# Optimization experiments

Measured on AMD Instinct MI355X. Metric: run time of the kernel, lower is better.

Reference implementation:

```python
import jax, jax.numpy as jnp
import numpy as np

INFEAT = 4096
OUTFEAT = 11008
TOKENS = 2048


def setup_inputs() -> dict:
    key = jax.random.key(0)
    k1, k2, k3, k4, k5 = jax.random.split(key, 5)
    x = jax.random.normal(k1, (TOKENS, INFEAT), dtype=jnp.float32)
    # Random uint8 int-weights, packed 4-per-uint32 exactly like pack():
    # word = w1 | w2<<8 | w3<<16 | w4<<24, rows grouped along infeatures.
    wbytes = jax.random.randint(k2, (INFEAT // 4, 4, OUTFEAT), 0, 256, dtype=jnp.int32).astype(jnp.uint32)
    qweight = (wbytes[:, 0] | (wbytes[:, 1] << 8) | (wbytes[:, 2] << 16) | (wbytes[:, 3] << 24))
    qweight = qweight.astype(jnp.int32)  # same bit pattern as uint32 buffer
    scales = (jax.random.uniform(k3, (OUTFEAT,), dtype=jnp.float32) * 0.01 + 1e-4)
    zeros = jax.random.randint(k4, (OUTFEAT,), 0, 256, dtype=jnp.int32)  # uint8 zero points
    bias = jax.random.normal(k5, (OUTFEAT,), dtype=jnp.float32) * 0.01
    return {"x": x, "qweight": qweight, "scales": scales, "zeros": zeros, "bias": bias}


def _dequant(qweight, scales, zeros):
    q = qweight.astype(jnp.uint32)  # [INFEAT//4, OUTFEAT]
    b0 = (q & 0xFF)
    b1 = ((q >> 8) & 0xFF)
    b2 = ((q >> 16) & 0xFF)
    b3 = ((q >> 24) & 0xFF)
    w_int = jnp.stack([b0, b1, b2, b3], axis=1).reshape(-1, q.shape[-1])  # [INFEAT, OUTFEAT]
    # pack(): int = round(w/scale) + zero  =>  w = (int - zero) * scale (per output channel)
    return (w_int.astype(jnp.float32) - zeros.astype(jnp.float32)[None, :]) * scales[None, :]


def reference(x, qweight, scales, zeros, bias):
    w = _dequant(qweight, scales, zeros)          # [INFEAT, OUTFEAT]
    return x @ w + bias[None, :]                  # [TOKENS, OUTFEAT]
```

## Files before the change

kernel.cpp:

```cpp
#include <hip/hip_runtime.h>
#include <hip/hip_bf16.h>

#define INFEAT 4096
#define OUTFEAT 11008
#define TOKENS 2048

typedef int v4i __attribute__((ext_vector_type(4)));
typedef __bf16 bf16_t;
typedef bf16_t bf16x4 __attribute__((ext_vector_type(4)));
typedef bf16_t bf16x8 __attribute__((ext_vector_type(8)));
typedef float f32x4 __attribute__((ext_vector_type(4)));

__device__ __forceinline__ void async_copy16(const void* g, void* l) {
    __builtin_amdgcn_global_load_lds((const __attribute__((address_space(1))) void*)g,
                                     (__attribute__((address_space(3))) void*)l,
                                     16, 0, 0);
}

__global__ __launch_bounds__(256) void quant_x(
    const float* __restrict__ x, unsigned int* __restrict__ xq,
    float* __restrict__ xscale, int* __restrict__ xsum)
{
    __shared__ float smax[4];
    __shared__ int ssum[4];
    const int row = blockIdx.x;
    const int tid = threadIdx.x;
    const int lane = tid & 63, wid = tid >> 6;
    const float* xr = x + (size_t)row * INFEAT;

    float4 v[4];
    #pragma unroll
    for (int i = 0; i < 4; ++i) v[i] = *(const float4*)&xr[tid * 16 + i * 4];

    float am = 0.f;
    #pragma unroll
    for (int i = 0; i < 4; ++i)
        am = fmaxf(am, fmaxf(fmaxf(fabsf(v[i].x), fabsf(v[i].y)),
                             fmaxf(fabsf(v[i].z), fabsf(v[i].w))));
    #pragma unroll
    for (int o = 32; o > 0; o >>= 1) am = fmaxf(am, __shfl_xor(am, o, 64));
    if (lane == 0) smax[wid] = am;
    __syncthreads();
    am = fmaxf(fmaxf(smax[0], smax[1]), fmaxf(smax[2], smax[3]));
    const float inv = am > 0.f ? 127.0f / am : 0.f;
    const float sc  = am > 0.f ? am / 127.0f : 0.f;

    int lsum = 0;
    unsigned int pk[4];
    #pragma unroll
    for (int i = 0; i < 4; ++i) {
        int q0 = (int)rintf(fminf(fmaxf(v[i].x * inv, -127.f), 127.f));
        int q1 = (int)rintf(fminf(fmaxf(v[i].y * inv, -127.f), 127.f));
        int q2 = (int)rintf(fminf(fmaxf(v[i].z * inv, -127.f), 127.f));
        int q3 = (int)rintf(fminf(fmaxf(v[i].w * inv, -127.f), 127.f));
        lsum += q0 + q1 + q2 + q3;
        pk[i] = (q0 & 255) | ((q1 & 255) << 8) | ((q2 & 255) << 16) | ((unsigned)(q3 & 255) << 24);
    }
    *(uint4*)&xq[(size_t)row * (INFEAT / 4) + tid * 4] = *(uint4*)pk;

    #pragma unroll
    for (int o = 32; o > 0; o >>= 1) lsum += __shfl_xor(lsum, o, 64);
    if (lane == 0) ssum[wid] = lsum;
    __syncthreads();
    if (tid == 0) {
        xsum[row] = ssum[0] + ssum[1] + ssum[2] + ssum[3];
        xscale[row] = sc;
    }
}

__global__ __launch_bounds__(256) void t_w(
    const unsigned int* __restrict__ qw, unsigned char* __restrict__ wt)
{
    __shared__ unsigned int Tw[64 * 64];
    const int n0 = blockIdx.x * 64;
    const int kp0 = blockIdx.y * 64;
    const int tn = threadIdx.x & 63;
    const int tk4 = threadIdx.x >> 6;

    #pragma unroll
    for (int it = 0; it < 16; ++it) {
        const int kp = tk4 * 16 + it;
        const unsigned int q = qw[(size_t)(kp0 + kp) * OUTFEAT + n0 + tn] ^ 0x80808080u;
        const int slot = (kp >> 2) ^ (tn & 15);
        Tw[tn * 64 + slot * 4 + (kp & 3)] = q;
    }
    __syncthreads();

    #pragma unroll
    for (int i = 0; i < 4; ++i) {
        const int flat = i * 256 + threadIdx.x;
        const int n = flat >> 4;
        const int c = flat & 15;
        uint4 v = *(const uint4*)&Tw[n * 64 + ((c ^ (n & 15)) * 4)];
        *(uint4*)&wt[(size_t)(n0 + n) * INFEAT + (size_t)kp0 * 4 + c * 16] = v;
    }
}

__global__ __launch_bounds__(256, 4) void q3gemm_i8(
    const unsigned char* __restrict__ xqb, const unsigned char* __restrict__ wt,
    const float* __restrict__ scales, const int* __restrict__ zeros,
    const float* __restrict__ bias, const float* __restrict__ xscale,
    const int* __restrict__ xsum, float* __restrict__ out)
{
    __shared__ unsigned char Als[128 * 128];
    __shared__ unsigned char Bls[128 * 128];

    const int tid = threadIdx.x;
    const int n0 = (blockIdx.x >> 4) * 128;
    const int m0 = (blockIdx.x & 15) * 128;

    const int wid = tid >> 6, lane = tid & 63;
    const int wm = (wid & 1) * 64, wn = (wid >> 1) * 64;
    const int lr = lane & 15, lq = lane >> 4;

    const int rb0  = wid * 32;
    const int rsub = lane >> 3;
    const int sl   = lane & 7;

    v4i acc[4][4];
    #pragma unroll
    for (int i = 0; i < 4; ++i)
        #pragma unroll
        for (int j = 0; j < 4; ++j)
            acc[i][j] = (v4i){0, 0, 0, 0};

    for (int kt = 0; kt < INFEAT / 128; ++kt) {
        const int k0 = kt * 128;

        #pragma unroll
        for (int p = 0; p < 4; ++p) {
            const int r = rb0 + p * 8 + rsub;
            const int s = sl ^ (r & 7);
            async_copy16(&xqb[(size_t)(m0 + r) * INFEAT + k0 + s * 16], Als + (rb0 + p * 8) * 128);
        }
        #pragma unroll
        for (int p = 0; p < 4; ++p) {
            const int r = rb0 + p * 8 + rsub;
            const int s = sl ^ (r & 7);
            async_copy16(&wt[(size_t)(n0 + r) * INFEAT + k0 + s * 16], Bls + (rb0 + p * 8) * 128);
        }

        __syncthreads();

        #pragma unroll
        for (int ks = 0; ks < 2; ++ks) {
            v4i af[4], bfv[4];
            #pragma unroll
            for (int t = 0; t < 4; ++t) {
                const int ra = wm + t * 16 + lr;
                const int pa = (ks * 4 + lq) ^ (ra & 7);
                af[t] = *(const v4i*)&Als[ra * 128 + pa * 16];
                const int rb = wn + t * 16 + lr;
                const int pb = (ks * 4 + lq) ^ (rb & 7);
                bfv[t] = *(const v4i*)&Bls[rb * 128 + pb * 16];
            }
            #pragma unroll
            for (int i = 0; i < 4; ++i)
                #pragma unroll
                for (int j = 0; j < 4; ++j)
                    acc[i][j] = __builtin_amdgcn_mfma_i32_16x16x64_i8(af[i], bfv[j], acc[i][j], 0, 0, 0);
        }

        __syncthreads();
    }

    #pragma unroll
    for (int j = 0; j < 4; ++j) {
        const int col = n0 + wn + j * 16 + lr;
        const float sn = scales[col];
        const int zi = 128 - zeros[col];
        const float bv = bias[col];
        #pragma unroll
        for (int i = 0; i < 4; ++i) {
            const int rb = m0 + wm + i * 16 + lq * 4;
            #pragma unroll
            for (int r = 0; r < 4; ++r) {
                const int tot = acc[i][j][r] + zi * xsum[rb + r];
                out[(size_t)(rb + r) * OUTFEAT + col] = xscale[rb + r] * sn * (float)tot + bv;
            }
        }
    }
}

#define LDSS 72
__global__ __launch_bounds__(256) void q3gemm_fb(
    const float* __restrict__ x, const unsigned int* __restrict__ qw,
    const float* __restrict__ scales, const int* __restrict__ zeros,
    const float* __restrict__ bias, float* __restrict__ out)
{
    __shared__ bf16_t Als[128 * LDSS];
    __shared__ bf16_t Bls[128 * LDSS];
    const int tid = threadIdx.x;
    const int m0 = blockIdx.y * 128;
    const int n0 = blockIdx.x * 128;
    const int bcol = tid & 127;
    const int bpr  = tid >> 7;
    const float scf = scales[n0 + bcol];
    const float nzs = (float)zeros[n0 + bcol] * scf;
    const int acolg = tid & 15;
    const int arow0 = tid >> 4;
    const int wid  = tid >> 6;
    const int lane = tid & 63;
    const int wm = (wid & 1) * 64;
    const int wn = (wid >> 1) * 64;
    const int lr = lane & 15;
    const int lq = lane >> 4;
    f32x4 acc[4][4];
    #pragma unroll
    for (int i = 0; i < 4; ++i)
        #pragma unroll
        for (int j = 0; j < 4; ++j) acc[i][j] = (f32x4)0.0f;
    for (int kt = 0; kt < INFEAT / 64; ++kt) {
        const int k0 = kt * 64;
        #pragma unroll
        for (int p = 0; p < 8; ++p) {
            const int row = arow0 + p * 16;
            const float4 v = *(const float4*)&x[(size_t)(m0 + row) * INFEAT + k0 + acolg * 4];
            bf16x4 b;
            b[0] = (bf16_t)v.x; b[1] = (bf16_t)v.y; b[2] = (bf16_t)v.z; b[3] = (bf16_t)v.w;
            *(bf16x4*)&Als[row * LDSS + acolg * 4] = b;
        }
        const int kp0 = k0 >> 2;
        #pragma unroll
        for (int it = 0; it < 8; ++it) {
            const int prel = it * 2 + bpr;
            const unsigned int q = qw[(size_t)(kp0 + prel) * OUTFEAT + n0 + bcol];
            bf16x4 b;
            b[0] = (bf16_t)((float)(q & 0xFFu)        * scf - nzs);
            b[1] = (bf16_t)((float)((q >> 8) & 0xFFu) * scf - nzs);
            b[2] = (bf16_t)((float)((q >> 16) & 0xFFu)* scf - nzs);
            b[3] = (bf16_t)((float)(q >> 24)          * scf - nzs);
            *(bf16x4*)&Bls[bcol * LDSS + prel * 4] = b;
        }
        __syncthreads();
        #pragma unroll
        for (int ks = 0; ks < 2; ++ks) {
            bf16x8 af[4], bfv[4];
            #pragma unroll
            for (int t = 0; t < 4; ++t) {
                af[t]  = *(const bf16x8*)&Als[(wm + t * 16 + lr) * LDSS + ks * 32 + lq * 8];
                bfv[t] = *(const bf16x8*)&Bls[(wn + t * 16 + lr) * LDSS + ks * 32 + lq * 8];
            }
            #pragma unroll
            for (int i = 0; i < 4; ++i)
                #pragma unroll
                for (int j = 0; j < 4; ++j)
                    acc[i][j] = __builtin_amdgcn_mfma_f32_16x16x32_bf16(af[i], bfv[j], acc[i][j], 0, 0, 0);
        }
        __syncthreads();
    }
    #pragma unroll
    for (int j = 0; j < 4; ++j) {
        const int col = n0 + wn + j * 16 + lr;
        const float bv = bias[col];
        #pragma unroll
        for (int i = 0; i < 4; ++i) {
            const int rbs = m0 + wm + i * 16 + lq * 4;
            #pragma unroll
            for (int r = 0; r < 4; ++r)
                out[(size_t)(rbs + r) * OUTFEAT + col] = acc[i][j][r] + bv;
        }
    }
}

extern "C" void kernel_launch(void* const* d_in, const int* in_sizes, int n_in,
                              void* d_out, int out_size, void* d_ws, size_t ws_size,
                              hipStream_t stream) {
    const float*        x      = (const float*)d_in[0];
    const unsigned int* qw     = (const unsigned int*)d_in[1];
    const float*        scales = (const float*)d_in[2];
    const int*          zeros  = (const int*)d_in[3];
    const float*        bias   = (const float*)d_in[4];
    float*              out    = (float*)d_out;

    const size_t wt_bytes = (size_t)OUTFEAT * INFEAT;
    const size_t xq_bytes = (size_t)TOKENS * INFEAT;
    const size_t need = wt_bytes + xq_bytes + TOKENS * (sizeof(float) + sizeof(int)) + 256;

    if (ws_size >= need) {
        unsigned char* wt = (unsigned char*)d_ws;
        unsigned int* xq  = (unsigned int*)((char*)d_ws + wt_bytes);
        float* xscale = (float*)((char*)d_ws + wt_bytes + xq_bytes);
        int*   xsum   = (int*)((char*)d_ws + wt_bytes + xq_bytes + TOKENS * sizeof(float));

        quant_x<<<dim3(TOKENS), dim3(256), 0, stream>>>(x, xq, xscale, xsum);
        t_w<<<dim3(OUTFEAT / 64, (INFEAT / 4) / 64), dim3(256), 0, stream>>>(qw, wt);
        q3gemm_i8<<<dim3((OUTFEAT / 128) * (TOKENS / 128)), dim3(256), 0, stream>>>(
            (const unsigned char*)xq, wt, scales, zeros, bias, xscale, xsum, out);
    } else {
        q3gemm_fb<<<dim3(OUTFEAT / 128, TOKENS / 128), dim3(256), 0, stream>>>(
            x, qw, scales, zeros, bias, out);
    }
}
```

Measured before the change: 297.6 us.

## Fuse weight transpose into int8 GEMM B-tile load, drop t_w kernel

Removes the separate weight transpose kernel and its 45MB workspace round trip. The GEMM now reads packed qweight words directly from global memory into registers, flips the sign bits, and writes them transposed into the swizzled LDS B tile. This saves one kernel launch and a full write plus re-read of the transposed weight. In exchange, B loads become synchronous register loads instead of async global-to-LDS copies, which adds latency and register pressure inside the main loop. The weight is also re-read and re-transposed by each of the 16 M-tiles.

```diff
diff --git a/kernel.cpp b/kernel.cpp
--- a/kernel.cpp
+++ b/kernel.cpp
@@ -68,36 +68,8 @@
     }
 }
 
-__global__ __launch_bounds__(256) void t_w(
-    const unsigned int* __restrict__ qw, unsigned char* __restrict__ wt)
-{
-    __shared__ unsigned int Tw[64 * 64];
-    const int n0 = blockIdx.x * 64;
-    const int kp0 = blockIdx.y * 64;
-    const int tn = threadIdx.x & 63;
-    const int tk4 = threadIdx.x >> 6;
-
-    #pragma unroll
-    for (int it = 0; it < 16; ++it) {
-        const int kp = tk4 * 16 + it;
-        const unsigned int q = qw[(size_t)(kp0 + kp) * OUTFEAT + n0 + tn] ^ 0x80808080u;
-        const int slot = (kp >> 2) ^ (tn & 15);
-        Tw[tn * 64 + slot * 4 + (kp & 3)] = q;
-    }
-    __syncthreads();
-
-    #pragma unroll
-    for (int i = 0; i < 4; ++i) {
-        const int flat = i * 256 + threadIdx.x;
-        const int n = flat >> 4;
-        const int c = flat & 15;
-        uint4 v = *(const uint4*)&Tw[n * 64 + ((c ^ (n & 15)) * 4)];
-        *(uint4*)&wt[(size_t)(n0 + n) * INFEAT + (size_t)kp0 * 4 + c * 16] = v;
-    }
-}
-
-__global__ __launch_bounds__(256, 4) void q3gemm_i8(
-    const unsigned char* __restrict__ xqb, const unsigned char* __restrict__ wt,
+__global__ __launch_bounds__(256, 4) void q3gemm_i8f(
+    const unsigned char* __restrict__ xqb, const unsigned int* __restrict__ qw,
     const float* __restrict__ scales, const int* __restrict__ zeros,
     const float* __restrict__ bias, const float* __restrict__ xscale,
     const int* __restrict__ xsum, float* __restrict__ out)
@@ -117,6 +89,9 @@
     const int rsub = lane >> 3;
     const int sl   = lane & 7;
 
+    const int bn  = tid & 127;
+    const int kph = tid >> 7;
+
     v4i acc[4][4];
     #pragma unroll
     for (int i = 0; i < 4; ++i)
@@ -125,7 +100,13 @@
             acc[i][j] = (v4i){0, 0, 0, 0};
 
     for (int kt = 0; kt < INFEAT / 128; ++kt) {
-        const int k0 = kt * 128;
+        const int k0  = kt * 128;
+        const int kp0 = kt * 32;
+
+        const unsigned int* bp = qw + (size_t)(kp0 + kph * 16) * OUTFEAT + n0 + bn;
+        unsigned int bq[16];
+        #pragma unroll
+        for (int w = 0; w < 16; ++w) bq[w] = bp[(size_t)w * OUTFEAT];
 
         #pragma unroll
         for (int p = 0; p < 4; ++p) {
@@ -133,11 +114,16 @@
             const int s = sl ^ (r & 7);
             async_copy16(&xqb[(size_t)(m0 + r) * INFEAT + k0 + s * 16], Als + (rb0 + p * 8) * 128);
         }
-        #pragma unroll
-        for (int p = 0; p < 4; ++p) {
-            const int r = rb0 + p * 8 + rsub;
-            const int s = sl ^ (r & 7);
-            async_copy16(&wt[(size_t)(n0 + r) * INFEAT + k0 + s * 16], Bls + (rb0 + p * 8) * 128);
+
+        #pragma unroll
+        for (int g = 0; g < 4; ++g) {
+            const int c = kph * 4 + g;
+            uint4 v;
+            v.x = bq[g * 4 + 0] ^ 0x80808080u;
+            v.y = bq[g * 4 + 1] ^ 0x80808080u;
+            v.z = bq[g * 4 + 2] ^ 0x80808080u;
+            v.w = bq[g * 4 + 3] ^ 0x80808080u;
+            *(uint4*)&Bls[bn * 128 + (c ^ (bn & 7)) * 16] = v;
         }
 
         __syncthreads();
@@ -273,20 +259,17 @@
     const float*        bias   = (const float*)d_in[4];
     float*              out    = (float*)d_out;
 
-    const size_t wt_bytes = (size_t)OUTFEAT * INFEAT;
     const size_t xq_bytes = (size_t)TOKENS * INFEAT;
-    const size_t need = wt_bytes + xq_bytes + TOKENS * (sizeof(float) + sizeof(int)) + 256;
+    const size_t need = xq_bytes + TOKENS * (sizeof(float) + sizeof(int)) + 256;
 
     if (ws_size >= need) {
-        unsigned char* wt = (unsigned char*)d_ws;
-        unsigned int* xq  = (unsigned int*)((char*)d_ws + wt_bytes);
-        float* xscale = (float*)((char*)d_ws + wt_bytes + xq_bytes);
-        int*   xsum   = (int*)((char*)d_ws + wt_bytes + xq_bytes + TOKENS * sizeof(float));
+        unsigned int* xq  = (unsigned int*)d_ws;
+        float* xscale = (float*)((char*)d_ws + xq_bytes);
+        int*   xsum   = (int*)((char*)d_ws + xq_bytes + TOKENS * sizeof(float));
 
         quant_x<<<dim3(TOKENS), dim3(256), 0, stream>>>(x, xq, xscale, xsum);
-        t_w<<<dim3(OUTFEAT / 64, (INFEAT / 4) / 64), dim3(256), 0, stream>>>(qw, wt);
-        q3gemm_i8<<<dim3((OUTFEAT / 128) * (TOKENS / 128)), dim3(256), 0, stream>>>(
-            (const unsigned char*)xq, wt, scales, zeros, bias, xscale, xsum, out);
+        q3gemm_i8f<<<dim3((OUTFEAT / 128) * (TOKENS / 128)), dim3(256), 0, stream>>>(
+            (const unsigned char*)xq, qw, scales, zeros, bias, xscale, xsum, out);
     } else {
         q3gemm_fb<<<dim3(OUTFEAT / 128, TOKENS / 128), dim3(256), 0, stream>>>(
             x, qw, scales, zeros, bias, out);
```

After: 318.6 us. 1.07x slower.

## Double-buffer int8 GEMM LDS tiles with async prefetch two stages ahead

Applied to the files above, without the earlier changes.

Converts the int8 MFMA GEMM main loop to a double-buffered LDS pipeline. Tile t+2 is prefetched asynchronously while tile t is computed, using explicit vmcnt and lgkmcnt waits and s_barrier instead of __syncthreads. LDS per block doubles to 64KB and launch bounds drop from 4 to 2 blocks per CU. This trades occupancy for overlap of global loads with MFMA work. All fragments are loaded into registers before the barrier, which raises register pressure.

```diff
diff --git a/kernel.cpp b/kernel.cpp
--- a/kernel.cpp
+++ b/kernel.cpp
@@ -96,14 +96,14 @@
     }
 }
 
-__global__ __launch_bounds__(256, 4) void q3gemm_i8(
+__global__ __launch_bounds__(256, 2) void q3gemm_i8d(
     const unsigned char* __restrict__ xqb, const unsigned char* __restrict__ wt,
     const float* __restrict__ scales, const int* __restrict__ zeros,
     const float* __restrict__ bias, const float* __restrict__ xscale,
     const int* __restrict__ xsum, float* __restrict__ out)
 {
-    __shared__ unsigned char Als[128 * 128];
-    __shared__ unsigned char Bls[128 * 128];
+    __shared__ unsigned char Als[2][128 * 128];
+    __shared__ unsigned char Bls[2][128 * 128];
 
     const int tid = threadIdx.x;
     const int n0 = (blockIdx.x >> 4) * 128;
@@ -124,45 +124,73 @@
         for (int j = 0; j < 4; ++j)
             acc[i][j] = (v4i){0, 0, 0, 0};
 
-    for (int kt = 0; kt < INFEAT / 128; ++kt) {
-        const int k0 = kt * 128;
-
-        #pragma unroll
-        for (int p = 0; p < 4; ++p) {
-            const int r = rb0 + p * 8 + rsub;
-            const int s = sl ^ (r & 7);
-            async_copy16(&xqb[(size_t)(m0 + r) * INFEAT + k0 + s * 16], Als + (rb0 + p * 8) * 128);
-        }
-        #pragma unroll
-        for (int p = 0; p < 4; ++p) {
-            const int r = rb0 + p * 8 + rsub;
-            const int s = sl ^ (r & 7);
-            async_copy16(&wt[(size_t)(n0 + r) * INFEAT + k0 + s * 16], Bls + (rb0 + p * 8) * 128);
-        }
-
-        __syncthreads();
-
-        #pragma unroll
-        for (int ks = 0; ks < 2; ++ks) {
-            v4i af[4], bfv[4];
-            #pragma unroll
-            for (int t = 0; t < 4; ++t) {
-                const int ra = wm + t * 16 + lr;
+#define STAGE(T, C) do {                                                              \
+    const int kk0_ = (T) * 128;                                                       \
+    _Pragma("unroll")                                                                 \
+    for (int p_ = 0; p_ < 4; ++p_) {                                                  \
+        const int r_ = rb0 + p_ * 8 + rsub;                                           \
+        const int s_ = sl ^ (r_ & 7);                                                 \
+        async_copy16(&xqb[(size_t)(m0 + r_) * INFEAT + kk0_ + s_ * 16],               \
+                     &Als[C][(rb0 + p_ * 8) * 128]);                                  \
+    }                                                                                 \
+    _Pragma("unroll")                                                                 \
+    for (int p_ = 0; p_ < 4; ++p_) {                                                  \
+        const int r_ = rb0 + p_ * 8 + rsub;                                           \
+        const int s_ = sl ^ (r_ & 7);                                                 \
+        async_copy16(&wt[(size_t)(n0 + r_) * INFEAT + kk0_ + s_ * 16],                \
+                     &Bls[C][(rb0 + p_ * 8) * 128]);                                  \
+    }                                                                                 \
+} while (0)
+
+    const int NT = INFEAT / 128;
+
+    STAGE(0, 0);
+    STAGE(1, 1);
+    asm volatile("s_waitcnt vmcnt(8)" ::: "memory");
+    __builtin_amdgcn_sched_barrier(0);
+    __builtin_amdgcn_s_barrier();
+    __builtin_amdgcn_sched_barrier(0);
+
+    for (int t = 0; t < NT; ++t) {
+        const int cur = t & 1;
+        const unsigned char* Ab = Als[cur];
+        const unsigned char* Bb = Bls[cur];
+
+        v4i af[2][4], bfv[2][4];
+        #pragma unroll
+        for (int ks = 0; ks < 2; ++ks)
+            #pragma unroll
+            for (int q = 0; q < 4; ++q) {
+                const int ra = wm + q * 16 + lr;
                 const int pa = (ks * 4 + lq) ^ (ra & 7);
-                af[t] = *(const v4i*)&Als[ra * 128 + pa * 16];
-                const int rb = wn + t * 16 + lr;
+                af[ks][q] = *(const v4i*)&Ab[ra * 128 + pa * 16];
+                const int rb = wn + q * 16 + lr;
                 const int pb = (ks * 4 + lq) ^ (rb & 7);
-                bfv[t] = *(const v4i*)&Bls[rb * 128 + pb * 16];
+                bfv[ks][q] = *(const v4i*)&Bb[rb * 128 + pb * 16];
             }
+        asm volatile("s_waitcnt lgkmcnt(0)" ::: "memory");
+        __builtin_amdgcn_sched_barrier(0);
+        __builtin_amdgcn_s_barrier();
+        __builtin_amdgcn_sched_barrier(0);
+
+        if (t + 2 < NT) STAGE(t + 2, cur);
+
+        #pragma unroll
+        for (int ks = 0; ks < 2; ++ks)
             #pragma unroll
             for (int i = 0; i < 4; ++i)
                 #pragma unroll
                 for (int j = 0; j < 4; ++j)
-                    acc[i][j] = __builtin_amdgcn_mfma_i32_16x16x64_i8(af[i], bfv[j], acc[i][j], 0, 0, 0);
-        }
-
-        __syncthreads();
-    }
+                    acc[i][j] = __builtin_amdgcn_mfma_i32_16x16x64_i8(af[ks][i], bfv[ks][j], acc[i][j], 0, 0, 0);
+
+        __builtin_amdgcn_sched_barrier(0);
+        if (t < NT - 2) { asm volatile("s_waitcnt vmcnt(8)" ::: "memory"); }
+        else            { asm volatile("s_waitcnt vmcnt(0)" ::: "memory"); }
+        __builtin_amdgcn_sched_barrier(0);
+        __builtin_amdgcn_s_barrier();
+        __builtin_amdgcn_sched_barrier(0);
+    }
+#undef STAGE
 
     #pragma unroll
     for (int j = 0; j < 4; ++j) {
@@ -285,7 +313,7 @@
 
         quant_x<<<dim3(TOKENS), dim3(256), 0, stream>>>(x, xq, xscale, xsum);
         t_w<<<dim3(OUTFEAT / 64, (INFEAT / 4) / 64), dim3(256), 0, stream>>>(qw, wt);
-        q3gemm_i8<<<dim3((OUTFEAT / 128) * (TOKENS / 128)), dim3(256), 0, stream>>>(
+        q3gemm_i8d<<<dim3((OUTFEAT / 128) * (TOKENS / 128)), dim3(256), 0, stream>>>(
             (const unsigned char*)xq, wt, scales, zeros, bias, xscale, xsum, out);
     } else {
         q3gemm_fb<<<dim3(OUTFEAT / 128, TOKENS / 128), dim3(256), 0, stream>>>(
```

New measurement: 267.1 us. -10.3%, faster.
